# Optimization experiments

Measured on AMD Instinct MI355X. Metric: run time of the kernel, lower is better.

The kernel has to match this reference:

```python
import jax, jax.numpy as jnp
import numpy as np

D_MODEL = 1024
N_HEADS = 16
D_EXP = 4
B, SQ, SKV = 2, 2048, 2048
LN_EPS = 1e-5


def _linear_params(key, d_in, d_out):
    kw, kb = jax.random.split(key)
    w = jax.random.normal(kw, (d_in, d_out), jnp.float32) * 0.02  # stored [in,out]
    b = jax.random.normal(kb, (d_out,), jnp.float32) * 0.02
    return w, b


def setup_inputs() -> dict:
    key = jax.random.key(0)
    ks = jax.random.split(key, 16)
    inp = {}
    inp["x"] = jax.random.normal(ks[0], (B, SQ, D_MODEL), jnp.float32)
    inp["encoder_out"] = jax.random.normal(ks[1], (B, SKV, D_MODEL), jnp.float32)
    # causal target mask, broadcast over batch and heads
    inp["tgt_mask"] = jnp.tril(jnp.ones((SQ, SQ), jnp.int32))[None, None]
    inp["src_mask"] = jnp.ones((1, 1, SQ, SKV), jnp.int32)
    # self-attention params
    inp["wq_s"], inp["bq_s"] = _linear_params(ks[2], D_MODEL, D_MODEL)
    inp["wk_s"], inp["bk_s"] = _linear_params(ks[3], D_MODEL, D_MODEL)
    inp["wv_s"], inp["bv_s"] = _linear_params(ks[4], D_MODEL, D_MODEL)
    inp["wo_s"], inp["bo_s"] = _linear_params(ks[5], D_MODEL, D_MODEL)
    # cross-attention params
    inp["wq_c"], inp["bq_c"] = _linear_params(ks[6], D_MODEL, D_MODEL)
    inp["wk_c"], inp["bk_c"] = _linear_params(ks[7], D_MODEL, D_MODEL)
    inp["wv_c"], inp["bv_c"] = _linear_params(ks[8], D_MODEL, D_MODEL)
    inp["wo_c"], inp["bo_c"] = _linear_params(ks[9], D_MODEL, D_MODEL)
    # feedforward params
    inp["ff1_w"], inp["ff1_b"] = _linear_params(ks[10], D_MODEL, D_MODEL * D_EXP)
    inp["ff2_w"], inp["ff2_b"] = _linear_params(ks[11], D_MODEL * D_EXP, D_MODEL)
    # layernorm params (3 AddNorms)
    for i, k in zip((1, 2, 3), (ks[12], ks[13], ks[14])):
        inp[f"ln{i}_g"] = jnp.ones((D_MODEL,), jnp.float32)
        inp[f"ln{i}_b"] = jnp.zeros((D_MODEL,), jnp.float32)
    return inp


def _layernorm(x, g, b):
    mu = jnp.mean(x, axis=-1, keepdims=True)
    var = jnp.mean(jnp.square(x - mu), axis=-1, keepdims=True)
    return (x - mu) / jnp.sqrt(var + LN_EPS) * g + b


def _mha(xq, xkv, wq, bq, wk, bk, wv, bv, wo, bo, mask):
    Bq, Sq, D = xq.shape
    Hd = D // N_HEADS
    q = (xq @ wq + bq).reshape(Bq, Sq, N_HEADS, Hd).transpose(0, 2, 1, 3)   # bhqd
    k = (xkv @ wk + bk).reshape(Bq, -1, N_HEADS, Hd).transpose(0, 2, 1, 3)  # bhkd
    v = (xkv @ wv + bv).reshape(Bq, -1, N_HEADS, Hd).transpose(0, 2, 1, 3)  # bhkd
    score = jnp.einsum("bhqd,bhkd->bhqk", q, k) / jnp.sqrt(jnp.float32(Hd))
    score = jnp.where(mask == 0, -jnp.inf, score)
    attn = jax.nn.softmax(score, axis=-1)
    ctx = jnp.einsum("bhqk,bhkd->bhqd", attn, v)
    ctx = ctx.transpose(0, 2, 1, 3).reshape(Bq, Sq, D)
    return ctx @ wo + bo


def reference(x, encoder_out, tgt_mask, src_mask,
              wq_s, bq_s, wk_s, bk_s, wv_s, bv_s, wo_s, bo_s,
              wq_c, bq_c, wk_c, bk_c, wv_c, bv_c, wo_c, bo_c,
              ff1_w, ff1_b, ff2_w, ff2_b,
              ln1_g, ln1_b, ln2_g, ln2_b, ln3_g, ln3_b):
    # dropout is identity in eval mode
    sa = _mha(x, x, wq_s, bq_s, wk_s, bk_s, wv_s, bv_s, wo_s, bo_s, tgt_mask)
    h = _layernorm(x + sa, ln1_g, ln1_b)
    ca = _mha(h, encoder_out, wq_c, bq_c, wk_c, bk_c, wv_c, bv_c, wo_c, bo_c, src_mask)
    h2 = _layernorm(h + ca, ln2_g, ln2_b)
    ff = jax.nn.relu(h2 @ ff1_w + ff1_b) @ ff2_w + ff2_b
    return _layernorm(h2 + ff, ln3_g, ln3_b)
```

## Files before the change

### kernel.cpp

```cpp
#include <hip/hip_runtime.h>
#include <stdint.h>

typedef __bf16 bf16;
typedef __attribute__((ext_vector_type(4))) float f32x4;
typedef __attribute__((ext_vector_type(8))) __bf16 bf16x8;
typedef __attribute__((ext_vector_type(4))) __bf16 bf16x4;
typedef __attribute__((ext_vector_type(4))) short s16x4;

#define DM   1024
#define NH   16
#define HDIM 64
#define BB   2
#define SEQ  2048
#define MR   (BB * SEQ)
#define DFF  4096
#define MEG  (1024 * 1024)

__global__ void detect_kernel(const unsigned int* __restrict__ xw,
                              int* __restrict__ flag) {
  int tid = threadIdx.x;
  int bad = 0;
  for (int i = tid; i < 4096; i += 64) {
    unsigned int w = xw[i];
    float flo = __uint_as_float((w & 0xffffu) << 16);
    if (!(fabsf(flo) < 100.f)) bad = 1;
  }
  unsigned long long m = __ballot(bad);
  if (tid == 0) *flag = (m == 0ull) ? 1 : 0;
}

__global__ __launch_bounds__(256) void cvt_big_kernel(
    const void* __restrict__ src, bf16* __restrict__ dst, int n4,
    const int* __restrict__ flag) {
  int i = blockIdx.x * 256 + threadIdx.x;
  if (i >= n4) return;
  if (*flag) {
    ((bf16x4*)dst)[i] = ((const bf16x4*)src)[i];
  } else {
    float4 v = ((const float4*)src)[i];
    bf16x4 o = {(bf16)v.x, (bf16)v.y, (bf16)v.z, (bf16)v.w};
    ((bf16x4*)dst)[i] = o;
  }
}

struct P16 { const void* p[16]; };
__global__ __launch_bounds__(256) void cvt_small_kernel(
    P16 ps, bf16* __restrict__ dstbase, const int* __restrict__ flag) {
  const int ncnt[16] = {1024,1024,1024,1024,1024,1024,1024,1024,
                        4096,1024,1024,1024,1024,1024,1024,1024};
  const int doff[16] = {0,1024,2048,3072,4096,5120,6144,7168,
                        8192,12288,13312,14336,15360,16384,17408,18432};
  int b = blockIdx.x;
  int n = ncnt[b];
  bool isbf = (*flag) != 0;
  const void* s = ps.p[b];
  bf16* d = dstbase + doff[b];
  for (int i = threadIdx.x; i * 4 < n; i += 256) {
    if (isbf) {
      ((bf16x4*)d)[i] = ((const bf16x4*)s)[i];
    } else {
      float4 v = ((const float4*)s)[i];
      bf16x4 o = {(bf16)v.x, (bf16)v.y, (bf16)v.z, (bf16)v.w};
      ((bf16x4*)d)[i] = o;
    }
  }
}

static __device__ __forceinline__ void gl_lds16(const bf16* g, bf16* l) {
  auto gp = reinterpret_cast<__attribute__((address_space(1))) unsigned int*>(
      reinterpret_cast<uintptr_t>(g));
  auto lp = reinterpret_cast<__attribute__((address_space(3))) unsigned int*>(
      (unsigned int)reinterpret_cast<uintptr_t>(l));
  __builtin_amdgcn_global_load_lds(gp, lp, 16, 0, 0);
}

static __device__ __forceinline__ s16x4 as_s16x4(bf16x4 v) {
  s16x4 r;
  __builtin_memcpy(&r, &v, 8);
  return r;
}

struct WTB {
  const void* src[10];
  int dstoff[10];
  int K[10], N[10];
  int bstart[10];
};
__global__ __launch_bounds__(256) void wt_all_kernel(WTB wb, bf16* __restrict__ wtbase,
                                                     const int* __restrict__ flag) {
  __shared__ alignas(16) bf16 tile[64][40];
  int bid = blockIdx.x;
  int wi = 0;
  while (wi < 9 && bid >= wb.bstart[wi + 1]) ++wi;
  int rel = bid - wb.bstart[wi];
  int N = wb.N[wi], K = wb.K[wi];
  int nb = N >> 6;
  int n0 = (rel % nb) * 64, k0 = (rel / nb) * 32;
  const void* w = wb.src[wi];
  bf16* wt = wtbase + wb.dstoff[wi];
  bool isbf = (*flag) != 0;
  int tid = threadIdx.x;
  int np = tid & 31, tk = tid >> 5;
#pragma unroll
  for (int i = 0; i < 4; ++i) {
    int kl = tk + i * 8;
    bf16 b0, b1;
    if (isbf) {
      unsigned int u = *(const unsigned int*)(
          (const bf16*)w + (size_t)(k0 + kl) * N + n0 + np * 2);
      unsigned short s0 = (unsigned short)(u & 0xffffu);
      unsigned short s1 = (unsigned short)(u >> 16);
      __builtin_memcpy(&b0, &s0, 2);
      __builtin_memcpy(&b1, &s1, 2);
    } else {
      const float* fp = (const float*)w + (size_t)(k0 + kl) * N + n0 + np * 2;
      b0 = (bf16)fp[0];
      b1 = (bf16)fp[1];
    }
    tile[np * 2][kl] = b0;
    tile[np * 2 + 1][kl] = b1;
  }
  __syncthreads();
  int nl = tid >> 2, kq = tid & 3;
  bf16x8 v = *(const bf16x8*)(&tile[nl][kq * 8]);
  *(bf16x8*)(wt + (size_t)(n0 + nl) * K + k0 + kq * 8) = v;
}

template <int TM>
__global__ __launch_bounds__(256) void gemm_kernel(
    const bf16* __restrict__ A, const bf16* __restrict__ Bt,
    const bf16* __restrict__ bias, bf16* __restrict__ outb,
    int M, int N, int K, int relu, int nbx) {
  constexpr int NI = TM / 32;
  constexpr int WM = TM / 2;
  constexpr int CA = TM / 64;
  __shared__ alignas(16) bf16 As[2][TM * 32];
  __shared__ alignas(16) bf16 Bs[2][128 * 32];
  int tid = threadIdx.x;
  int lane = tid & 63, wv = tid >> 6;
  int quad = lane >> 4, l15 = lane & 15;
  int wg = blockIdx.x;
  int w = (wg & 7) * (gridDim.x >> 3) + (wg >> 3);
  int bx = w % nbx, by = w / nbx;
  int m0 = by * TM, n0 = bx * 128;
  int wm = wv >> 1, wn = wv & 1;

  f32x4 acc[NI][4];
#pragma unroll
  for (int i = 0; i < NI; ++i)
#pragma unroll
    for (int j = 0; j < 4; ++j) acc[i][j] = (f32x4){0.f, 0.f, 0.f, 0.f};

  int sr = lane >> 2, sc = (lane & 3) * 8;
  const bf16* gA[CA];
  bf16* lA0[CA];
  bf16* lA1[CA];
#pragma unroll
  for (int t = 0; t < CA; ++t) {
    int ch = wv * CA + t;
    gA[t] = A + (size_t)(m0 + ch * 16 + sr) * K + sc;
    lA0[t] = As[0] + ch * 512 + lane * 8;
    lA1[t] = As[1] + ch * 512 + lane * 8;
  }
  const bf16* gB0 = Bt + (size_t)(n0 + (wv * 2) * 16 + sr) * K + sc;
  const bf16* gB1 = Bt + (size_t)(n0 + (wv * 2 + 1) * 16 + sr) * K + sc;
  bf16* lB00 = Bs[0] + (wv * 2) * 512 + lane * 8;
  bf16* lB01 = Bs[1] + (wv * 2) * 512 + lane * 8;
  bf16* lB10 = Bs[0] + (wv * 2 + 1) * 512 + lane * 8;
  bf16* lB11 = Bs[1] + (wv * 2 + 1) * 512 + lane * 8;

  for (int k0 = 0; k0 < K; k0 += 64) {
#pragma unroll
    for (int t = 0; t < CA; ++t) {
      gl_lds16(gA[t] + k0, lA0[t]);
      gl_lds16(gA[t] + k0 + 32, lA1[t]);
    }
    gl_lds16(gB0 + k0, lB00);
    gl_lds16(gB0 + k0 + 32, lB01);
    gl_lds16(gB1 + k0, lB10);
    gl_lds16(gB1 + k0 + 32, lB11);
    __syncthreads();
#pragma unroll
    for (int s = 0; s < 2; ++s) {
      bf16x8 af[NI], bfr[4];
#pragma unroll
      for (int i = 0; i < NI; ++i)
        af[i] = *(const bf16x8*)(As[s] + (wm * WM + i * 16 + l15) * 32 + quad * 8);
#pragma unroll
      for (int j = 0; j < 4; ++j)
        bfr[j] = *(const bf16x8*)(Bs[s] + (wn * 64 + j * 16 + l15) * 32 + quad * 8);
#pragma unroll
      for (int i = 0; i < NI; ++i)
#pragma unroll
        for (int j = 0; j < 4; ++j)
          acc[i][j] = __builtin_amdgcn_mfma_f32_16x16x32_bf16(af[i], bfr[j],
                                                              acc[i][j], 0, 0, 0);
    }
    __syncthreads();
  }

#pragma unroll
  for (int j = 0; j < 4; ++j) {
    int col = n0 + wn * 64 + j * 16 + l15;
    float bval = (float)bias[col];
#pragma unroll
    for (int i = 0; i < NI; ++i) {
      int rb = m0 + wm * WM + i * 16 + quad * 4;
#pragma unroll
      for (int r = 0; r < 4; ++r) {
        float v = acc[i][j][r] + bval;
        if (relu) v = fmaxf(v, 0.f);
        outb[(size_t)(rb + r) * N + col] = (bf16)v;
      }
    }
  }
}

__global__ __launch_bounds__(256) void gemm_splitk_kernel(
    const bf16* __restrict__ A, const bf16* __restrict__ Bt,
    float* __restrict__ pout, int M, int N, int KC, int Ktot, int nbx) {
  __shared__ alignas(16) bf16 As[2][128 * 32];
  __shared__ alignas(16) bf16 Bs[2][128 * 32];
  int tid = threadIdx.x;
  int lane = tid & 63, wv = tid >> 6;
  int quad = lane >> 4, l15 = lane & 15;
  int wg = blockIdx.x;
  int w = (wg & 7) * (gridDim.x >> 3) + (wg >> 3);
  int nxy = nbx * (M >> 7);
  int bz = w / nxy;
  int rem = w - bz * nxy;
  int bx = rem % nbx, by = rem / nbx;
  int m0 = by * 128, n0 = bx * 128;
  int wm = wv >> 1, wn = wv & 1;
  int kb = bz * KC;
  pout += (size_t)bz * M * N;

  f32x4 acc[4][4];
#pragma unroll
  for (int i = 0; i < 4; ++i)
#pragma unroll
    for (int j = 0; j < 4; ++j) acc[i][j] = (f32x4){0.f, 0.f, 0.f, 0.f};

  int sr = lane >> 2, sc = (lane & 3) * 8;
  const bf16* gA0 = A + (size_t)(m0 + (wv * 2) * 16 + sr) * Ktot + sc;
  const bf16* gA1 = A + (size_t)(m0 + (wv * 2 + 1) * 16 + sr) * Ktot + sc;
  const bf16* gB0 = Bt + (size_t)(n0 + (wv * 2) * 16 + sr) * Ktot + sc;
  const bf16* gB1 = Bt + (size_t)(n0 + (wv * 2 + 1) * 16 + sr) * Ktot + sc;
  bf16* lA00 = As[0] + (wv * 2) * 512 + lane * 8;
  bf16* lA01 = As[1] + (wv * 2) * 512 + lane * 8;
  bf16* lA10 = As[0] + (wv * 2 + 1) * 512 + lane * 8;
  bf16* lA11 = As[1] + (wv * 2 + 1) * 512 + lane * 8;
  bf16* lB00 = Bs[0] + (wv * 2) * 512 + lane * 8;
  bf16* lB01 = Bs[1] + (wv * 2) * 512 + lane * 8;
  bf16* lB10 = Bs[0] + (wv * 2 + 1) * 512 + lane * 8;
  bf16* lB11 = Bs[1] + (wv * 2 + 1) * 512 + lane * 8;

  for (int k0 = kb; k0 < kb + KC; k0 += 64) {
    gl_lds16(gA0 + k0, lA00);
    gl_lds16(gA0 + k0 + 32, lA01);
    gl_lds16(gA1 + k0, lA10);
    gl_lds16(gA1 + k0 + 32, lA11);
    gl_lds16(gB0 + k0, lB00);
    gl_lds16(gB0 + k0 + 32, lB01);
    gl_lds16(gB1 + k0, lB10);
    gl_lds16(gB1 + k0 + 32, lB11);
    __syncthreads();
#pragma unroll
    for (int s = 0; s < 2; ++s) {
      bf16x8 af[4], bfr[4];
#pragma unroll
      for (int i = 0; i < 4; ++i)
        af[i] = *(const bf16x8*)(As[s] + (wm * 64 + i * 16 + l15) * 32 + quad * 8);
#pragma unroll
      for (int j = 0; j < 4; ++j)
        bfr[j] = *(const bf16x8*)(Bs[s] + (wn * 64 + j * 16 + l15) * 32 + quad * 8);
#pragma unroll
      for (int i = 0; i < 4; ++i)
#pragma unroll
        for (int j = 0; j < 4; ++j)
          acc[i][j] = __builtin_amdgcn_mfma_f32_16x16x32_bf16(af[i], bfr[j],
                                                              acc[i][j], 0, 0, 0);
    }
    __syncthreads();
  }
#pragma unroll
  for (int j = 0; j < 4; ++j) {
    int col = n0 + wn * 64 + j * 16 + l15;
#pragma unroll
    for (int i = 0; i < 4; ++i) {
      int rb = m0 + wm * 64 + i * 16 + quad * 4;
#pragma unroll
      for (int r = 0; r < 4; ++r)
        pout[(size_t)(rb + r) * N + col] = acc[i][j][r];
    }
  }
}

__global__ __launch_bounds__(256) void vt_pre_kernel(
    const bf16* __restrict__ v, int vstride, bf16* __restrict__ vt, int skv) {
  __shared__ bf16 tile[32][33];
  int tid = threadIdx.x;
  int tx = tid & 31, ty = tid >> 5;
  int kv0 = blockIdx.x * 32, d0 = blockIdx.y * 32;
  int bh = blockIdx.z;
  int b = bh >> 4, h = bh & 15;
  const bf16* src = v + (size_t)b * skv * vstride + h * HDIM;
#pragma unroll
  for (int i = 0; i < 4; ++i)
    tile[ty + i * 8][tx] = src[(size_t)(kv0 + ty + i * 8) * vstride + d0 + tx];
  __syncthreads();
  bf16* dst = vt + ((size_t)bh * HDIM + d0) * skv + kv0;
#pragma unroll
  for (int i = 0; i < 4; ++i)
    dst[(size_t)(ty + i * 8) * skv + tx] = tile[tx][ty + i * 8];
}

__global__ __launch_bounds__(256, 4) void flash9_kernel(
    const bf16* __restrict__ Q, int qstride,
    const bf16* __restrict__ Kk, int kstride,
    const bf16* __restrict__ VT, bf16* __restrict__ ctx,
    float* __restrict__ opart, float* __restrict__ lpart,
    int skv, int causal, int nsplit) {
  __shared__ alignas(16) bf16 KTl[2][64 * 64];
  __shared__ alignas(16) bf16 VTl[2][64 * 64];
  int tid = threadIdx.x;
  int lane = tid & 63, wv = tid >> 6, quad = lane >> 4, l15 = lane & 15;
  int wg = blockIdx.x;
  int cpx = gridDim.x >> 3;
  int w = (wg & 7) * cpx + (wg >> 3);
  int qb = w & 15;
  int h = (w >> 4) & 15;
  int zz = w >> 8;
  int b = zz / nsplit;
  int half = zz - b * nsplit;
  int q0 = qb * 128;
  int qw = q0 + wv * 32;
  int l7 = l15 & 7;

  bf16x8 qf[2][2];
  const float qsc = 0.125f * 1.44269504f;
#pragma unroll
  for (int a = 0; a < 2; ++a) {
    const bf16* qp = Q + (size_t)(b * SEQ + qw + a * 16 + l15) * qstride + h * HDIM;
    qf[a][0] = *(const bf16x8*)(qp + quad * 8);
    qf[a][1] = *(const bf16x8*)(qp + 32 + quad * 8);
#pragma unroll
    for (int j = 0; j < 8; ++j) {
      qf[a][0][j] = (bf16)((float)qf[a][0][j] * qsc);
      qf[a][1][j] = (bf16)((float)qf[a][1][j] * qsc);
    }
  }
  s16x4 onesA = {0x3F80, 0x3F80, 0x3F80, 0x3F80};

  f32x4 o[2][4], oL[2];
#pragma unroll
  for (int a = 0; a < 2; ++a) {
    oL[a] = (f32x4){0.f, 0.f, 0.f, 0.f};
#pragma unroll
    for (int j = 0; j < 4; ++j) o[a][j] = (f32x4){0.f, 0.f, 0.f, 0.f};
  }

  int nch_tot = causal ? (q0 + 128) / 64 : skv / 64;
  int c_lo = (half * nch_tot) / nsplit;
  int c_hi = ((half + 1) * nch_tot) / nsplit;

  int l8 = lane >> 3;
  int colseg = (lane & 7) ^ l8;
  int grow = wv * 16 + l8;
  const bf16* kbase = Kk + ((size_t)b * skv + grow) * kstride + h * HDIM + colseg * 8;
  const bf16* vbase = VT + ((size_t)(b * NH + h) * HDIM + grow) * skv + colseg * 8;
  bf16* kls = &KTl[0][wv * 1024];
  bf16* vls = &VTl[0][wv * 1024];

  auto STAGE = [&](int bb, int cc) {
    const bf16* ks = kbase + (size_t)(cc * 64) * kstride;
    const bf16* vs = vbase + cc * 64;
    bf16* kd = kls + bb * 4096;
    bf16* vd = vls + bb * 4096;
    gl_lds16(ks, kd);
    gl_lds16(ks + (size_t)8 * kstride, kd + 512);
    gl_lds16(vs, vd);
    gl_lds16(vs + (size_t)8 * skv, vd + 512);
  };

  if (c_lo < c_hi) STAGE(0, c_lo);

  for (int c = c_lo; c < c_hi; ++c) {
    int cur = (c - c_lo) & 1;
    int kv0 = c * 64;
    __syncthreads();
    if (c + 1 < c_hi) STAGE(cur ^ 1, c + 1);

    if (!causal || kv0 <= qw + 31) {
      const bf16* kt_base = &KTl[0][0] + cur * 4096;
      const bf16* vt_base = &VTl[0][0] + cur * 4096;
      bf16x4 p[2][4];
#pragma unroll
      for (int t = 0; t < 4; ++t) {
        const bf16* kb = kt_base + (t * 16 + l15) * 64;
        bf16x8 kt0 = *(const bf16x8*)(kb + ((quad ^ l7) << 3));
        bf16x8 kt1 = *(const bf16x8*)(kb + (((quad + 4) ^ l7) << 3));
#pragma unroll
        for (int a = 0; a < 2; ++a) {
          f32x4 z = (f32x4){0.f, 0.f, 0.f, 0.f};
          z = __builtin_amdgcn_mfma_f32_16x16x32_bf16(kt0, qf[a][0], z, 0, 0, 0);
          z = __builtin_amdgcn_mfma_f32_16x16x32_bf16(kt1, qf[a][1], z, 0, 0, 0);
          if (causal && kv0 + 63 > qw) {
#pragma unroll
            for (int r = 0; r < 4; ++r)
              if (kv0 + t * 16 + quad * 4 + r > qw + a * 16 + l15)
                z[r] = -1e30f;
          }
          bf16x4 pk;
#pragma unroll
          for (int r = 0; r < 4; ++r) pk[r] = (bf16)exp2f(z[r]);
          p[a][t] = pk;
          oL[a] = __builtin_amdgcn_mfma_f32_16x16x16bf16_1k(
              onesA, as_s16x4(pk), oL[a], 0, 0, 0);
        }
      }
#pragma unroll
      for (int jt = 0; jt < 4; ++jt) {
        const bf16* vb = vt_base + (jt * 16 + l15) * 64;
        bf16x4 af[4];
#pragma unroll
        for (int t = 0; t < 4; ++t)
          af[t] = *(const bf16x4*)(
              vb + ((((t * 2 + (quad >> 1)) ^ l7) << 3) + ((quad & 1) << 2)));
#pragma unroll
        for (int a = 0; a < 2; ++a)
#pragma unroll
          for (int t = 0; t < 4; ++t)
            o[a][jt] = __builtin_amdgcn_mfma_f32_16x16x16bf16_1k(
                as_s16x4(af[t]), as_s16x4(p[a][t]), o[a][jt], 0, 0, 0);
      }
    }
  }

  if (nsplit == 1) {
#pragma unroll
    for (int a = 0; a < 2; ++a) {
      float inv = 1.0f / fmaxf(oL[a][0], 1e-30f);
      bf16* cp = ctx + (size_t)(b * SEQ + qw + a * 16 + l15) * DM + h * HDIM + quad * 4;
#pragma unroll
      for (int jt = 0; jt < 4; ++jt) {
        bf16x4 ob = {(bf16)(o[a][jt][0] * inv), (bf16)(o[a][jt][1] * inv),
                     (bf16)(o[a][jt][2] * inv), (bf16)(o[a][jt][3] * inv)};
        *(bf16x4*)(cp + jt * 16) = ob;
      }
    }
  } else {
#pragma unroll
    for (int a = 0; a < 2; ++a) {
      float* op = opart + (size_t)half * MR * DM +
                  (size_t)(b * SEQ + qw + a * 16 + l15) * DM + h * HDIM + quad * 4;
#pragma unroll
      for (int jt = 0; jt < 4; ++jt) *(f32x4*)(op + jt * 16) = o[a][jt];
      if (lane < 16)
        lpart[(size_t)((half * BB + b) * NH + h) * SEQ + qw + a * 16 + l15] =
            oL[a][0];
    }
  }
}

template <int NS>
__global__ __launch_bounds__(256) void flash_comb_kernel(
    const float* __restrict__ opart, const float* __restrict__ lpart,
    bf16* __restrict__ ctx) {
  int row = blockIdx.x, tid = threadIdx.x;
  int b = row >> 11, q = row & (SEQ - 1);
  int h = tid >> 4;
  float l = 0.f;
#pragma unroll
  for (int s = 0; s < NS; ++s)
    l += lpart[(size_t)((s * BB + b) * NH + h) * SEQ + q];
  float inv = 1.0f / fmaxf(l, 1e-30f);
  float a0 = 0.f, a1 = 0.f, a2 = 0.f, a3 = 0.f;
#pragma unroll
  for (int s = 0; s < NS; ++s) {
    f32x4 v = ((const f32x4*)(opart + (size_t)s * MR * DM + (size_t)row * DM))[tid];
    a0 += v[0]; a1 += v[1]; a2 += v[2]; a3 += v[3];
  }
  bf16x4 ob = {(bf16)(a0 * inv), (bf16)(a1 * inv),
               (bf16)(a2 * inv), (bf16)(a3 * inv)};
  ((bf16x4*)(ctx + (size_t)row * DM))[tid] = ob;
}

template <int NP>
__global__ __launch_bounds__(256) void addnorm_red_kernel(
    const bf16* __restrict__ res, const float* __restrict__ part,
    const bf16* __restrict__ bias, const bf16* __restrict__ g,
    const bf16* __restrict__ be, bf16* __restrict__ yb,
    void* __restrict__ outAny, const int* __restrict__ flag) {
  int row = blockIdx.x, tid = threadIdx.x;
  float a0 = 0.f, a1 = 0.f, a2 = 0.f, a3 = 0.f;
#pragma unroll
  for (int p = 0; p < NP; ++p) {
    float4 v = ((const float4*)(part + (size_t)p * MR * DM + (size_t)row * DM))[tid];
    a0 += v.x; a1 += v.y; a2 += v.z; a3 += v.w;
  }
  bf16x4 bb = ((const bf16x4*)bias)[tid];
  bf16x4 rr = ((const bf16x4*)(res + (size_t)row * DM))[tid];
  float s0 = (float)rr[0] + a0 + (float)bb[0];
  float s1 = (float)rr[1] + a1 + (float)bb[1];
  float s2 = (float)rr[2] + a2 + (float)bb[2];
  float s3 = (float)rr[3] + a3 + (float)bb[3];
  float sum = s0 + s1 + s2 + s3;
  float sq = s0 * s0 + s1 * s1 + s2 * s2 + s3 * s3;
#pragma unroll
  for (int mk = 32; mk >= 1; mk >>= 1) {
    sum += __shfl_xor(sum, mk, 64);
    sq += __shfl_xor(sq, mk, 64);
  }
  __shared__ float red[8];
  int wvi = tid >> 6, lane = tid & 63;
  if (lane == 0) { red[wvi * 2] = sum; red[wvi * 2 + 1] = sq; }
  __syncthreads();
  sum = red[0] + red[2] + red[4] + red[6];
  sq = red[1] + red[3] + red[5] + red[7];
  float mu = sum * (1.0f / DM);
  float var = sq * (1.0f / DM) - mu * mu;
  float rstd = rsqrtf(var + 1e-5f);
  bf16x4 g4 = ((const bf16x4*)g)[tid];
  bf16x4 b4 = ((const bf16x4*)be)[tid];
  float y0 = (s0 - mu) * rstd * (float)g4[0] + (float)b4[0];
  float y1 = (s1 - mu) * rstd * (float)g4[1] + (float)b4[1];
  float y2 = (s2 - mu) * rstd * (float)g4[2] + (float)b4[2];
  float y3 = (s3 - mu) * rstd * (float)g4[3] + (float)b4[3];
  if (yb) {
    bf16x4 ob = {(bf16)y0, (bf16)y1, (bf16)y2, (bf16)y3};
    ((bf16x4*)(yb + (size_t)row * DM))[tid] = ob;
  }
  if (outAny) {
    if (*flag) {
      bf16x4 ob = {(bf16)y0, (bf16)y1, (bf16)y2, (bf16)y3};
      ((bf16x4*)outAny)[(size_t)row * 256 + tid] = ob;
    } else {
      ((float4*)outAny)[(size_t)row * 256 + tid] = make_float4(y0, y1, y2, y3);
    }
  }
}

extern "C" void kernel_launch(void* const* d_in, const int* in_sizes, int n_in,
                              void* d_out, int out_size, void* d_ws, size_t ws_size,
                              hipStream_t stream) {
  (void)in_sizes; (void)n_in; (void)out_size; (void)ws_size;
  const void* x_raw   = d_in[0];
  const void* enc_raw = d_in[1];

  char* ws = (char*)d_ws;
  size_t off = 0;
  auto alloc = [&](size_t bytes) -> void* {
    void* p = ws + off;
    off += (bytes + 255) & ~(size_t)255;
    return p;
  };
  const size_t SB = (size_t)MR * DM;
  int* flag    = (int*)alloc(256);
  bf16* smallb = (bf16*)alloc(20480 * 2);
  bf16* wt   = (bf16*)alloc((size_t)16 * MEG * 2);
  bf16* xb   = (bf16*)alloc(SB * 2);
  bf16* encb = (bf16*)alloc(SB * 2);
  bf16* vtg  = (bf16*)alloc(SB * 2);
  bf16* ctx  = (bf16*)alloc(SB * 2);
  bf16* hb1  = (bf16*)alloc(SB * 2);
  bf16* hb2  = (bf16*)alloc(SB * 2);
  bf16* qkv  = (bf16*)alloc(SB * 3 * 2);
  bf16* kvc  = (bf16*)alloc(SB * 2 * 2);
  float* part = (float*)alloc(SB * 4 * 4);
  float* lpart = (float*)alloc((size_t)3 * BB * NH * SEQ * 4);
  bf16* gbuf = qkv;
  bf16* qc   = xb;

  bf16* b_qkvs = smallb + 0;     bf16* b_os  = smallb + 3072;
  bf16* b_qc   = smallb + 4096;  bf16* b_kvc = smallb + 5120;
  bf16* b_oc   = smallb + 7168;  bf16* b_f1  = smallb + 8192;
  bf16* b_f2   = smallb + 12288;
  bf16* l1g = smallb + 13312; bf16* l1b = smallb + 14336;
  bf16* l2g = smallb + 15360; bf16* l2b = smallb + 16384;
  bf16* l3g = smallb + 17408; bf16* l3b = smallb + 18432;

  detect_kernel<<<1, 64, 0, stream>>>((const unsigned int*)x_raw, flag);
  cvt_big_kernel<<<(int)(SB / 1024), 256, 0, stream>>>(x_raw, xb, (int)(SB / 4), flag);
  cvt_big_kernel<<<(int)(SB / 1024), 256, 0, stream>>>(enc_raw, encb, (int)(SB / 4), flag);
  P16 ps;
  ps.p[0] = d_in[5];  ps.p[1] = d_in[7];  ps.p[2] = d_in[9];  ps.p[3] = d_in[11];
  ps.p[4] = d_in[13]; ps.p[5] = d_in[15]; ps.p[6] = d_in[17]; ps.p[7] = d_in[19];
  ps.p[8] = d_in[21]; ps.p[9] = d_in[23];
  ps.p[10] = d_in[24]; ps.p[11] = d_in[25]; ps.p[12] = d_in[26];
  ps.p[13] = d_in[27]; ps.p[14] = d_in[28]; ps.p[15] = d_in[29];
  cvt_small_kernel<<<16, 256, 0, stream>>>(ps, smallb, flag);

  WTB wb;
  const int wsrc[10] = {4, 6, 8, 10, 12, 14, 16, 18, 20, 22};
  for (int i = 0; i < 10; ++i) {
    wb.src[i] = d_in[wsrc[i]];
    wb.K[i] = 1024; wb.N[i] = 1024;
    wb.dstoff[i] = i * MEG;
  }
  wb.N[8] = 4096;
  wb.K[9] = 4096; wb.dstoff[9] = 12 * MEG;
  int bacc = 0;
  for (int i = 0; i < 10; ++i) {
    wb.bstart[i] = bacc;
    bacc += (wb.N[i] / 64) * (wb.K[i] / 32);
  }
  wt_all_kernel<<<bacc, 256, 0, stream>>>(wb, wt, flag);

  gemm_kernel<128><<<24 * 32, 256, 0, stream>>>(xb, wt, b_qkvs, qkv,
                                                MR, 3072, DM, 0, 24);
  vt_pre_kernel<<<dim3(SEQ / 32, 2, 32), 256, 0, stream>>>(qkv + 2048, 3072, vtg, SEQ);
  flash9_kernel<<<16 * 16 * BB * 2, 256, 0, stream>>>(
      qkv, 3072, qkv + 1024, 3072, vtg, ctx, part, lpart, SEQ, 1, 2);
  flash_comb_kernel<2><<<MR, 256, 0, stream>>>(part, lpart, ctx);
  gemm_splitk_kernel<<<8 * 32 * 2, 256, 0, stream>>>(
      ctx, wt + (size_t)3 * MEG, part, MR, DM, 512, DM, 8);
  addnorm_red_kernel<2><<<MR, 256, 0, stream>>>(xb, part, b_os, l1g, l1b,
                                                hb1, nullptr, flag);
  gemm_kernel<64><<<8 * 64, 256, 0, stream>>>(hb1, wt + (size_t)4 * MEG,
                                              b_qc, qc, MR, DM, DM, 0, 8);
  gemm_kernel<128><<<16 * 32, 256, 0, stream>>>(encb, wt + (size_t)5 * MEG,
                                                b_kvc, kvc, MR, 2048, DM, 0, 16);
  vt_pre_kernel<<<dim3(SEQ / 32, 2, 32), 256, 0, stream>>>(kvc + 1024, 2048, vtg, SEQ);
  flash9_kernel<<<16 * 16 * BB * 2, 256, 0, stream>>>(
      qc, 1024, kvc, 2048, vtg, ctx, part, lpart, SEQ, 0, 2);
  flash_comb_kernel<2><<<MR, 256, 0, stream>>>(part, lpart, ctx);
  gemm_splitk_kernel<<<8 * 32 * 2, 256, 0, stream>>>(
      ctx, wt + (size_t)7 * MEG, part, MR, DM, 512, DM, 8);
  addnorm_red_kernel<2><<<MR, 256, 0, stream>>>(hb1, part, b_oc, l2g, l2b,
                                                hb2, nullptr, flag);
  gemm_kernel<128><<<32 * 32, 256, 0, stream>>>(hb2, wt + (size_t)8 * MEG,
                                                b_f1, gbuf, MR, DFF, DM, 1, 32);
  gemm_splitk_kernel<<<8 * 32 * 4, 256, 0, stream>>>(
      gbuf, wt + (size_t)12 * MEG, part, MR, DM, 1024, DFF, 8);
  addnorm_red_kernel<4><<<MR, 256, 0, stream>>>(hb2, part, b_f2, l3g, l3b,
                                                nullptr, d_out, flag);
}
```

Measured before the change: 636.0 us.

## Single-buffer flash LDS, raise occupancy to 8, and split KV four ways

Replaces the double-buffered K/V LDS staging in the flash attention kernel with a single buffer guarded by two barriers per chunk. This halves LDS use, and the launch bound is raised to 8 waves-groups per CU. The KV split factor goes from 2 to 4, which doubles the grid, and the combine kernel and lpart buffer are sized to match. The aim is more parallelism and occupancy to hide latency. In exchange the kernel loses its load/compute overlap inside a block, does more partial-output combine work, and must fit tighter register limits.

```diff
diff --git a/kernel.cpp b/kernel.cpp
--- a/kernel.cpp
+++ b/kernel.cpp
@@ -315,14 +315,14 @@
     dst[(size_t)(ty + i * 8) * skv + tx] = tile[tx][ty + i * 8];
 }
 
-__global__ __launch_bounds__(256, 4) void flash9_kernel(
+__global__ __launch_bounds__(256, 8) void flash11_kernel(
     const bf16* __restrict__ Q, int qstride,
     const bf16* __restrict__ Kk, int kstride,
     const bf16* __restrict__ VT, bf16* __restrict__ ctx,
     float* __restrict__ opart, float* __restrict__ lpart,
     int skv, int causal, int nsplit) {
-  __shared__ alignas(16) bf16 KTl[2][64 * 64];
-  __shared__ alignas(16) bf16 VTl[2][64 * 64];
+  __shared__ alignas(16) bf16 KTl[64 * 64];
+  __shared__ alignas(16) bf16 VTl[64 * 64];
   int tid = threadIdx.x;
   int lane = tid & 63, wv = tid >> 6, quad = lane >> 4, l15 = lane & 15;
   int wg = blockIdx.x;
@@ -369,35 +369,29 @@
   int grow = wv * 16 + l8;
   const bf16* kbase = Kk + ((size_t)b * skv + grow) * kstride + h * HDIM + colseg * 8;
   const bf16* vbase = VT + ((size_t)(b * NH + h) * HDIM + grow) * skv + colseg * 8;
-  bf16* kls = &KTl[0][wv * 1024];
-  bf16* vls = &VTl[0][wv * 1024];
-
-  auto STAGE = [&](int bb, int cc) {
+  bf16* kls = &KTl[wv * 1024];
+  bf16* vls = &VTl[wv * 1024];
+
+  auto STAGE = [&](int cc) {
     const bf16* ks = kbase + (size_t)(cc * 64) * kstride;
     const bf16* vs = vbase + cc * 64;
-    bf16* kd = kls + bb * 4096;
-    bf16* vd = vls + bb * 4096;
-    gl_lds16(ks, kd);
-    gl_lds16(ks + (size_t)8 * kstride, kd + 512);
-    gl_lds16(vs, vd);
-    gl_lds16(vs + (size_t)8 * skv, vd + 512);
+    gl_lds16(ks, kls);
+    gl_lds16(ks + (size_t)8 * kstride, kls + 512);
+    gl_lds16(vs, vls);
+    gl_lds16(vs + (size_t)8 * skv, vls + 512);
   };
 
-  if (c_lo < c_hi) STAGE(0, c_lo);
-
   for (int c = c_lo; c < c_hi; ++c) {
-    int cur = (c - c_lo) & 1;
     int kv0 = c * 64;
     __syncthreads();
-    if (c + 1 < c_hi) STAGE(cur ^ 1, c + 1);
+    STAGE(c);
+    __syncthreads();
 
     if (!causal || kv0 <= qw + 31) {
-      const bf16* kt_base = &KTl[0][0] + cur * 4096;
-      const bf16* vt_base = &VTl[0][0] + cur * 4096;
       bf16x4 p[2][4];
 #pragma unroll
       for (int t = 0; t < 4; ++t) {
-        const bf16* kb = kt_base + (t * 16 + l15) * 64;
+        const bf16* kb = KTl + (t * 16 + l15) * 64;
         bf16x8 kt0 = *(const bf16x8*)(kb + ((quad ^ l7) << 3));
         bf16x8 kt1 = *(const bf16x8*)(kb + (((quad + 4) ^ l7) << 3));
 #pragma unroll
@@ -421,7 +415,7 @@
       }
 #pragma unroll
       for (int jt = 0; jt < 4; ++jt) {
-        const bf16* vb = vt_base + (jt * 16 + l15) * 64;
+        const bf16* vb = VTl + (jt * 16 + l15) * 64;
         bf16x4 af[4];
 #pragma unroll
         for (int t = 0; t < 4; ++t)
@@ -568,7 +562,7 @@
   bf16* qkv  = (bf16*)alloc(SB * 3 * 2);
   bf16* kvc  = (bf16*)alloc(SB * 2 * 2);
   float* part = (float*)alloc(SB * 4 * 4);
-  float* lpart = (float*)alloc((size_t)3 * BB * NH * SEQ * 4);
+  float* lpart = (float*)alloc((size_t)4 * BB * NH * SEQ * 4);
   bf16* gbuf = qkv;
   bf16* qc   = xb;
 
@@ -610,9 +604,9 @@
   gemm_kernel<128><<<24 * 32, 256, 0, stream>>>(xb, wt, b_qkvs, qkv,
                                                 MR, 3072, DM, 0, 24);
   vt_pre_kernel<<<dim3(SEQ / 32, 2, 32), 256, 0, stream>>>(qkv + 2048, 3072, vtg, SEQ);
-  flash9_kernel<<<16 * 16 * BB * 2, 256, 0, stream>>>(
-      qkv, 3072, qkv + 1024, 3072, vtg, ctx, part, lpart, SEQ, 1, 2);
-  flash_comb_kernel<2><<<MR, 256, 0, stream>>>(part, lpart, ctx);
+  flash11_kernel<<<16 * 16 * BB * 4, 256, 0, stream>>>(
+      qkv, 3072, qkv + 1024, 3072, vtg, ctx, part, lpart, SEQ, 1, 4);
+  flash_comb_kernel<4><<<MR, 256, 0, stream>>>(part, lpart, ctx);
   gemm_splitk_kernel<<<8 * 32 * 2, 256, 0, stream>>>(
       ctx, wt + (size_t)3 * MEG, part, MR, DM, 512, DM, 8);
   addnorm_red_kernel<2><<<MR, 256, 0, stream>>>(xb, part, b_os, l1g, l1b,
@@ -622,9 +616,9 @@
   gemm_kernel<128><<<16 * 32, 256, 0, stream>>>(encb, wt + (size_t)5 * MEG,
                                                 b_kvc, kvc, MR, 2048, DM, 0, 16);
   vt_pre_kernel<<<dim3(SEQ / 32, 2, 32), 256, 0, stream>>>(kvc + 1024, 2048, vtg, SEQ);
-  flash9_kernel<<<16 * 16 * BB * 2, 256, 0, stream>>>(
-      qc, 1024, kvc, 2048, vtg, ctx, part, lpart, SEQ, 0, 2);
-  flash_comb_kernel<2><<<MR, 256, 0, stream>>>(part, lpart, ctx);
+  flash11_kernel<<<16 * 16 * BB * 4, 256, 0, stream>>>(
+      qc, 1024, kvc, 2048, vtg, ctx, part, lpart, SEQ, 0, 4);
+  flash_comb_kernel<4><<<MR, 256, 0, stream>>>(part, lpart, ctx);
   gemm_splitk_kernel<<<8 * 32 * 2, 256, 0, stream>>>(
       ctx, wt + (size_t)7 * MEG, part, MR, DM, 512, DM, 8);
   addnorm_red_kernel<2><<<MR, 256, 0, stream>>>(hb1, part, b_oc, l2g, l2b,
```

Result: slower. 1.121 ms (+76.2%).
